# Kernel optimization log

Measured on AMD Instinct MI355X. Metric: run time of the kernel, lower is better.

Reference implementation:

```python
import jax, jax.numpy as jnp
import numpy as np

H = 8  # head_num

def setup_inputs() -> dict:
    key = jax.random.key(0)
    k1, k2, k3, k4, k5 = jax.random.split(key, 5)
    n, e = 4096, 128
    x = jax.random.normal(k1, (n, e), dtype=jnp.float32)
    # torch Linear weights stored here as [in, out]; scale ~ 1/sqrt(fan_in)
    w_qkv = jax.random.normal(k2, (e, e * 3 * H), dtype=jnp.float32) * (1.0 / np.sqrt(e))
    b_qkv = jax.random.normal(k3, (e * 3 * H,), dtype=jnp.float32) * 0.01
    w_proj = jax.random.normal(k4, (e * H, e), dtype=jnp.float32) * (1.0 / np.sqrt(e * H))
    b_proj = jax.random.normal(k5, (e,), dtype=jnp.float32) * 0.01
    return {"x": x, "w_qkv": w_qkv, "b_qkv": b_qkv, "w_proj": w_proj, "b_proj": b_proj}

def reference(x, w_qkv, b_qkv, w_proj, b_proj):
    n, e = x.shape
    # packed layout along output dim is (h, d, qkv) per rearrange 'n (h d qkv) -> qkv h n d'
    qkv = (x @ w_qkv + b_qkv).reshape(n, H, e, 3)          # [n, h, d, 3]
    q = jnp.transpose(qkv[..., 0], (1, 0, 2))              # [h, n, d]
    k = jnp.transpose(qkv[..., 1], (1, 0, 2))
    v = jnp.transpose(qkv[..., 2], (1, 0, 2))
    energy = jnp.einsum('hqd,hkd->hqk', q, k)              # [h, n, n]
    scaling = jnp.asarray(e, x.dtype) ** 0.5
    att = jax.nn.softmax(energy, axis=-1) / scaling        # post-softmax scale (as in source)
    out = jnp.einsum('hqk,hkd->hqd', att, v)               # [h, n, d]
    out = jnp.transpose(out, (1, 0, 2)).reshape(n, H * e)  # [n, h*d]
    return out @ w_proj + b_proj
```

## Files before the change

### kernel.cpp

```cpp
#include <hip/hip_runtime.h>
#include <hip/hip_fp16.h>


#define N_TOK 4096
#define DH 128
#define NH 8

#define EXP2F(x) __builtin_amdgcn_exp2f(x)

typedef _Float16 f16;
typedef __attribute__((ext_vector_type(8))) _Float16 f16x8;
typedef __attribute__((ext_vector_type(2))) __fp16 hf2;
typedef __attribute__((ext_vector_type(4))) float f32x4;

#define GLD16(gsrc, ldst) __builtin_amdgcn_global_load_lds( \
    (const __attribute__((address_space(1))) void*)(gsrc), \
    (__attribute__((address_space(3))) void*)(ldst), 16, 0, 0)

__global__ __launch_bounds__(256) void conv_weights(
    const float* __restrict__ w_proj, const float* __restrict__ w_qkv,
    const float* __restrict__ b_qkv,
    f16* __restrict__ wpT, f16* __restrict__ wqkvT, float* __restrict__ bperm)
{
  int t = blockIdx.x * 256 + threadIdx.x;
  if (t < 131072) {
    int k = t >> 7, col = t & 127;
    wpT[col * 1024 + k] = (f16)w_proj[t];
  } else {
    t -= 131072;
    int k = t / 3072;
    int col = t - k * 3072;
    int hh = col / 384;
    int rem = col - hh * 384;
    int d = rem / 3;
    int s = rem - d * 3;
    int colp = s * 1024 + hh * 128 + d;
    float scale = (s == 0) ? 1.4426950408889634f : 1.0f;
    wqkvT[colp * 128 + k] = (f16)(w_qkv[t] * scale);
    if (k == 0) bperm[colp] = b_qkv[col] * scale;
  }
}

__global__ __launch_bounds__(256) void qkv_gemm2(
    const float* __restrict__ x, const f16* __restrict__ wqkvT,
    const float* __restrict__ bperm,
    f16* __restrict__ Qh, f16* __restrict__ Kh, f16* __restrict__ Vt)
{
  const int cb = blockIdx.x;
  const int rb = blockIdx.y;
  const int tid = threadIdx.x;
  const int w = tid >> 6, lane = tid & 63;
  const int l16 = lane & 15, lhi = lane >> 4;
  const int s = cb >> 3, h = cb & 7;

  f16x8 xf[2][4];
#pragma unroll
  for (int m = 0; m < 2; ++m)
#pragma unroll
    for (int kt = 0; kt < 4; ++kt) {
      const float* xp = x + (size_t)(rb * 128 + w * 32 + m * 16 + l16) * 128 + kt * 32 + lhi * 8;
      f32x4 x0 = *(const f32x4*)xp, x1 = *(const f32x4*)(xp + 4);
      f16x8 v;
#pragma unroll
      for (int j = 0; j < 4; ++j) { v[j] = (f16)x0[j]; v[4 + j] = (f16)x1[j]; }
      xf[m][kt] = v;
    }

  f32x4 acc[8][2];
#pragma unroll
  for (int nt = 0; nt < 8; ++nt)
#pragma unroll
    for (int m = 0; m < 2; ++m) acc[nt][m] = (f32x4){0.f, 0.f, 0.f, 0.f};

#pragma unroll
  for (int nt = 0; nt < 8; ++nt)
#pragma unroll
    for (int kt = 0; kt < 4; ++kt) {
      f16x8 wf = *(const f16x8*)(wqkvT + (size_t)(cb * 128 + nt * 16 + l16) * 128 + kt * 32 + lhi * 8);
      acc[nt][0] = __builtin_amdgcn_mfma_f32_16x16x32_f16(wf, xf[0][kt], acc[nt][0], 0, 0, 0);
      acc[nt][1] = __builtin_amdgcn_mfma_f32_16x16x32_f16(wf, xf[1][kt], acc[nt][1], 0, 0, 0);
    }

#pragma unroll
  for (int nt = 0; nt < 8; ++nt) {
    f32x4 bb = *(const f32x4*)(bperm + cb * 128 + nt * 16 + 4 * lhi);
#pragma unroll
    for (int m = 0; m < 2; ++m) acc[nt][m] += bb;
  }

  if (s == 2) {
#pragma unroll
    for (int nt = 0; nt < 8; ++nt)
#pragma unroll
      for (int m = 0; m < 2; ++m)
#pragma unroll
        for (int r = 0; r < 4; ++r)
          Vt[(size_t)(h * 128 + nt * 16 + 4 * lhi + r) * N_TOK + rb * 128 + w * 32 + m * 16 + l16] =
              (f16)acc[nt][m][r];
  } else {
    __shared__ f16 tr[128][136];
#pragma unroll
    for (int nt = 0; nt < 8; ++nt)
#pragma unroll
      for (int m = 0; m < 2; ++m)
#pragma unroll
        for (int r = 0; r < 4; ++r)
          tr[w * 32 + m * 16 + l16][nt * 16 + 4 * lhi + r] = (f16)acc[nt][m][r];
    __syncthreads();
    f16* dst = (s == 0 ? Qh : Kh) + (size_t)(h * N_TOK + rb * 128) * 128;
    int r = tid >> 1, dh = (tid & 1) * 64;
#pragma unroll
    for (int i = 0; i < 8; ++i)
      *(f16x8*)(dst + r * 128 + dh + i * 8) = *(const f16x8*)(&tr[r][dh + i * 8]);
  }
}

__global__ __launch_bounds__(512, 2) void flash_attn(
    const f16* __restrict__ Qh, const f16* __restrict__ Kh,
    const f16* __restrict__ Vt, f16* __restrict__ opart, float* __restrict__ mlpart)
{
  const int bid = blockIdx.x;
  const int h = bid & 7, sp = (bid >> 3) & 1, qb = bid >> 4;
  const int tid = threadIdx.x;
  const int w = tid >> 6, lane = tid & 63;
  const int l16 = lane & 15, lhi = lane >> 4;

  __shared__ __align__(16) char smem[65536];

  f16x8 qf[2][4];
#pragma unroll
  for (int m = 0; m < 2; ++m)
#pragma unroll
    for (int kt = 0; kt < 4; ++kt)
      qf[m][kt] = *(const f16x8*)(Qh +
          (size_t)(h * N_TOK + qb * 256 + w * 32 + m * 16 + l16) * DH + kt * 32 + lhi * 8);

  int koff[4][4], voff[2][8];
#pragma unroll
  for (int nt = 0; nt < 4; ++nt) {
    int row = 32 * (nt >> 1) + 8 * (l16 >> 2) + 4 * (nt & 1) + (l16 & 3);
    int fk = (row & 3) | ((row & 8) >> 1);
#pragma unroll
    for (int kt = 0; kt < 4; ++kt)
      koff[nt][kt] = row * 256 + ((kt * 4 + lhi) ^ fk) * 16;
  }
#pragma unroll
  for (int ks = 0; ks < 2; ++ks)
#pragma unroll
    for (int dt = 0; dt < 8; ++dt) {
      int rowv = dt * 16 + l16;
      voff[ks][dt] = rowv * 128 + (((ks * 4 + lhi) ^ (rowv & 7))) * 16;
    }

  f32x4 o[2][8];
#pragma unroll
  for (int m = 0; m < 2; ++m)
#pragma unroll
    for (int dt = 0; dt < 8; ++dt) o[m][dt] = (f32x4){0.f, 0.f, 0.f, 0.f};
  float mrun[2] = {-3e38f, -3e38f}, lrun[2] = {0.f, 0.f};

  const f16* Kgh = Kh + (size_t)h * N_TOK * DH;
  const f16* Vgh = Vt + (size_t)h * DH * N_TOK;

  auto stage = [&](int buf, int kb) {
    char* kd = smem + buf * 16384;
    char* vd = smem + 32768 + buf * 16384;
#pragma unroll
    for (int c2 = 0; c2 < 2; ++c2) {
      int c = w * 2 + c2;
      {
        int row = c * 4 + (lane >> 4);
        int fk = (row & 3) | ((row & 8) >> 1);
        const f16* src = Kgh + (size_t)(kb * 64 + row) * DH + ((lane & 15) ^ fk) * 8;
        GLD16(src, kd + c * 1024);
      }
      {
        int row = c * 8 + (lane >> 3);
        const f16* src = Vgh + (size_t)row * N_TOK + kb * 64 + ((lane & 7) ^ (row & 7)) * 8;
        GLD16(src, vd + c * 1024);
      }
    }
  };

  const int kb0 = sp * 32;
  stage(0, kb0);
  asm volatile("s_waitcnt vmcnt(0)" ::: "memory");
  __builtin_amdgcn_sched_barrier(0);
  __builtin_amdgcn_s_barrier();

  int buf = 0;
  for (int kb = kb0; kb < kb0 + 32; ++kb) {
    if (kb < kb0 + 31) {
      stage(buf ^ 1, kb + 1);
      asm volatile("s_waitcnt vmcnt(4)" ::: "memory");
    } else {
      asm volatile("s_waitcnt vmcnt(0)" ::: "memory");
    }
    __builtin_amdgcn_sched_barrier(0);
    __builtin_amdgcn_s_barrier();

    const char* kd = smem + buf * 16384;
    const char* vd = smem + 32768 + buf * 16384;

    f32x4 sv[2][4];
    __builtin_amdgcn_s_setprio(1);
#pragma unroll
    for (int nt = 0; nt < 4; ++nt) {
      f32x4 a0 = {0.f, 0.f, 0.f, 0.f}, a1 = {0.f, 0.f, 0.f, 0.f};
#pragma unroll
      for (int kt = 0; kt < 4; ++kt) {
        f16x8 kf = *(const f16x8*)(kd + koff[nt][kt]);
        a0 = __builtin_amdgcn_mfma_f32_16x16x32_f16(kf, qf[0][kt], a0, 0, 0, 0);
        a1 = __builtin_amdgcn_mfma_f32_16x16x32_f16(kf, qf[1][kt], a1, 0, 0, 0);
      }
      sv[0][nt] = a0; sv[1][nt] = a1;
    }
    __builtin_amdgcn_s_setprio(0);

    f16x8 pf[2][2];
#pragma unroll
    for (int m = 0; m < 2; ++m) {
      f32x4 mv;
#pragma unroll
      for (int r = 0; r < 4; ++r)
        mv[r] = fmaxf(fmaxf(sv[m][0][r], sv[m][1][r]), fmaxf(sv[m][2][r], sv[m][3][r]));
      float pmax = fmaxf(fmaxf(mv[0], mv[1]), fmaxf(mv[2], mv[3]));
      if (!__all(pmax - mrun[m] <= 8.f)) {
        float rm = fmaxf(pmax, __shfl_xor(pmax, 16));
        rm = fmaxf(rm, __shfl_xor(rm, 32));
        float mnew = fmaxf(mrun[m], rm);
        float sc = EXP2F(mrun[m] - mnew);
        lrun[m] *= sc;
#pragma unroll
        for (int dt = 0; dt < 8; ++dt) o[m][dt] *= sc;
        mrun[m] = mnew;
      }
      float mr = mrun[m];
      f32x4 ps = {0.f, 0.f, 0.f, 0.f};
#pragma unroll
      for (int nt = 0; nt < 4; ++nt)
#pragma unroll
        for (int r = 0; r < 4; ++r) {
          float p = EXP2F(sv[m][nt][r] - mr);
          sv[m][nt][r] = p;
          ps[r] += p;
        }
      lrun[m] += (ps[0] + ps[1]) + (ps[2] + ps[3]);
#pragma unroll
      for (int ks = 0; ks < 2; ++ks) {
        union { f16x8 v; hf2 hh[4]; } u;
        u.hh[0] = __builtin_amdgcn_cvt_pkrtz(sv[m][2 * ks][0], sv[m][2 * ks][1]);
        u.hh[1] = __builtin_amdgcn_cvt_pkrtz(sv[m][2 * ks][2], sv[m][2 * ks][3]);
        u.hh[2] = __builtin_amdgcn_cvt_pkrtz(sv[m][2 * ks + 1][0], sv[m][2 * ks + 1][1]);
        u.hh[3] = __builtin_amdgcn_cvt_pkrtz(sv[m][2 * ks + 1][2], sv[m][2 * ks + 1][3]);
        pf[m][ks] = u.v;
      }
    }

    __builtin_amdgcn_s_setprio(1);
#pragma unroll
    for (int ks = 0; ks < 2; ++ks)
#pragma unroll
      for (int dt = 0; dt < 8; ++dt) {
        f16x8 vf = *(const f16x8*)(vd + voff[ks][dt]);
        o[0][dt] = __builtin_amdgcn_mfma_f32_16x16x32_f16(vf, pf[0][ks], o[0][dt], 0, 0, 0);
        o[1][dt] = __builtin_amdgcn_mfma_f32_16x16x32_f16(vf, pf[1][ks], o[1][dt], 0, 0, 0);
      }
    __builtin_amdgcn_s_setprio(0);

    __builtin_amdgcn_s_barrier();
    buf ^= 1;
  }

  f16* ob = opart + ((size_t)((sp * 8 + h) * 16 + qb)) * 32768;
  float* mlb = mlpart + ((size_t)((sp * 8 + h) * 16 + qb)) * 512;
#pragma unroll
  for (int m = 0; m < 2; ++m) {
    float lr = lrun[m];
    lr += __shfl_xor(lr, 16);
    lr += __shfl_xor(lr, 32);
    float rl = 1.0f / lr;
#pragma unroll
    for (int dt = 0; dt < 8; ++dt)
#pragma unroll
      for (int r = 0; r < 4; ++r)
        ob[(dt * 16 + 4 * lhi + r) * 256 + w * 32 + m * 16 + l16] = (f16)(o[m][dt][r] * rl);
    if (lhi == 0) {
      mlb[w * 32 + m * 16 + l16] = mrun[m];
      mlb[256 + w * 32 + m * 16 + l16] = lr;
    }
  }
}

__global__ __launch_bounds__(256) void proj_combine(
    const f16* __restrict__ opart, const float* __restrict__ mlpart,
    const f16* __restrict__ wpT, const float* __restrict__ b_proj,
    float* __restrict__ out)
{
  const int tid = threadIdx.x;
  const int w = tid >> 6;
  const int lane = tid & 63;
  const int l16 = lane & 15, lhi = lane >> 4;
  const int rb = blockIdx.x * 16;
  const int qb = rb >> 8;
  const int nl0 = rb & 255;

  __shared__ f16 A[16][1032];
  __shared__ float wl[8][16][3];
  __shared__ float red[4][16][128];

  const float isc = 0.08838834764831845f;
  if (tid < 128) {
    int hh = tid >> 4, n = tid & 15;
    const float* ml0 = mlpart + ((size_t)((0 + hh) * 16 + qb)) * 512 + nl0 + n;
    const float* ml1 = mlpart + ((size_t)((8 + hh) * 16 + qb)) * 512 + nl0 + n;
    float m0 = ml0[0], l0 = ml0[256], m1 = ml1[0], l1 = ml1[256];
    float mt = fmaxf(m0, m1);
    float n0 = EXP2F(m0 - mt) * l0, n1 = EXP2F(m1 - mt) * l1;
    wl[hh][n][0] = n0; wl[hh][n][1] = n1;
    wl[hh][n][2] = isc / (n0 + n1);
  }
  __syncthreads();

  {
    int d = tid >> 1, nn = (tid & 1) * 8;
#pragma unroll
    for (int hh = 0; hh < 8; ++hh) {
      const f16* O0 = opart + ((size_t)((0 + hh) * 16 + qb)) * 32768 + d * 256 + nl0 + nn;
      const f16* O1 = opart + ((size_t)((8 + hh) * 16 + qb)) * 32768 + d * 256 + nl0 + nn;
      f16x8 a0 = *(const f16x8*)O0, a1 = *(const f16x8*)O1;
#pragma unroll
      for (int j = 0; j < 8; ++j) {
        int n = nn + j;
        float v = ((float)a0[j] * wl[hh][n][0] + (float)a1[j] * wl[hh][n][1]) * wl[hh][n][2];
        A[n][hh * 128 + d] = (f16)v;
      }
    }
  }
  __syncthreads();

  f32x4 o[8];
#pragma unroll
  for (int dt = 0; dt < 8; ++dt) o[dt] = (f32x4){0.f, 0.f, 0.f, 0.f};

#pragma unroll
  for (int kb = 0; kb < 8; ++kb) {
    int k0 = w * 256 + kb * 32 + lhi * 8;
    f16x8 a = *(const f16x8*)(&A[l16][k0]);
#pragma unroll
    for (int dt = 0; dt < 8; ++dt) {
      f16x8 b = *(const f16x8*)(wpT + (size_t)(dt * 16 + l16) * 1024 + k0);
      o[dt] = __builtin_amdgcn_mfma_f32_16x16x32_f16(a, b, o[dt], 0, 0, 0);
    }
  }

#pragma unroll
  for (int dt = 0; dt < 8; ++dt)
#pragma unroll
    for (int r = 0; r < 4; ++r)
      red[w][lhi * 4 + r][dt * 16 + l16] = o[dt][r];
  __syncthreads();
#pragma unroll
  for (int i = 0; i < 8; ++i) {
    int idx = tid + 256 * i;
    int row = idx >> 7, col = idx & 127;
    float v = red[0][row][col] + red[1][row][col] + red[2][row][col]
            + red[3][row][col] + b_proj[col];
    out[(size_t)(rb + row) * 128 + col] = v;
  }
}

extern "C" void kernel_launch(void* const* d_in, const int* in_sizes, int n_in,
                              void* d_out, int out_size, void* d_ws, size_t ws_size,
                              hipStream_t stream) {
  const float* x      = (const float*)d_in[0];
  const float* w_qkv  = (const float*)d_in[1];
  const float* b_qkv  = (const float*)d_in[2];
  const float* w_proj = (const float*)d_in[3];
  const float* b_proj = (const float*)d_in[4];
  float* out = (float*)d_out;

  char* ws = (char*)d_ws;
  const size_t MB = 1024 * 1024;
  f16*   Qh     = (f16*)(ws);
  f16*   Kh     = (f16*)(ws + 8 * MB);
  f16*   Vt     = (f16*)(ws + 16 * MB);
  f16*   opart  = (f16*)(ws + 24 * MB);
  float* mlpart = (float*)(ws + 40 * MB);
  f16*   wpT    = (f16*)(ws + 40 * MB + 512 * 1024);
  f16*   wqkvT  = (f16*)(ws + 40 * MB + 768 * 1024);
  float* bperm  = (float*)(ws + 41 * MB + 512 * 1024);

  hipLaunchKernelGGL(conv_weights, dim3(2048), dim3(256), 0, stream,
                     w_proj, w_qkv, b_qkv, wpT, wqkvT, bperm);
  hipLaunchKernelGGL(qkv_gemm2, dim3(24, 32), dim3(256), 0, stream,
                     x, wqkvT, bperm, Qh, Kh, Vt);
  hipLaunchKernelGGL(flash_attn, dim3(256), dim3(512), 0, stream,
                     Qh, Kh, Vt, opart, mlpart);
  hipLaunchKernelGGL(proj_combine, dim3(256), dim3(256), 0, stream,
                     opart, mlpart, wpT, b_proj, out);
}
```

Baseline: 137.1 us.

## Split attention KV range four ways and trade double buffering for occupancy

The flash attention kernel now splits the key range into four chunks instead of two, doubling the grid to 512 blocks. It drops the double-buffered LDS pipeline for a single 32 KB buffer with plain syncthreads, and raises the launch-bounds occupancy hint from 2 to 4, so more blocks share a CU and hide latency instead of explicit prefetch. The projection/combine kernel merges four partial softmax results instead of two, and the workspace layout grows to hold the larger partial output. The risks are register pressure or spills under the tighter occupancy hint, no load/compute overlap within a block, and extra partial traffic in the combine step.

```diff
diff --git a/kernel.cpp b/kernel.cpp
--- a/kernel.cpp
+++ b/kernel.cpp
@@ -115,17 +115,17 @@
   }
 }
 
-__global__ __launch_bounds__(512, 2) void flash_attn(
+__global__ __launch_bounds__(512, 4) void flash_attn(
     const f16* __restrict__ Qh, const f16* __restrict__ Kh,
     const f16* __restrict__ Vt, f16* __restrict__ opart, float* __restrict__ mlpart)
 {
   const int bid = blockIdx.x;
-  const int h = bid & 7, sp = (bid >> 3) & 1, qb = bid >> 4;
+  const int h = bid & 7, sp = (bid >> 3) & 3, qb = bid >> 5;
   const int tid = threadIdx.x;
   const int w = tid >> 6, lane = tid & 63;
   const int l16 = lane & 15, lhi = lane >> 4;
 
-  __shared__ __align__(16) char smem[65536];
+  __shared__ __align__(16) char smem[32768];
 
   f16x8 qf[2][4];
 #pragma unroll
@@ -162,9 +162,9 @@
   const f16* Kgh = Kh + (size_t)h * N_TOK * DH;
   const f16* Vgh = Vt + (size_t)h * DH * N_TOK;
 
-  auto stage = [&](int buf, int kb) {
-    char* kd = smem + buf * 16384;
-    char* vd = smem + 32768 + buf * 16384;
+  auto stage = [&](int kb) {
+    char* kd = smem;
+    char* vd = smem + 16384;
 #pragma unroll
     for (int c2 = 0; c2 < 2; ++c2) {
       int c = w * 2 + c2;
@@ -182,25 +182,13 @@
     }
   };
 
-  const int kb0 = sp * 32;
-  stage(0, kb0);
-  asm volatile("s_waitcnt vmcnt(0)" ::: "memory");
-  __builtin_amdgcn_sched_barrier(0);
-  __builtin_amdgcn_s_barrier();
-
-  int buf = 0;
-  for (int kb = kb0; kb < kb0 + 32; ++kb) {
-    if (kb < kb0 + 31) {
-      stage(buf ^ 1, kb + 1);
-      asm volatile("s_waitcnt vmcnt(4)" ::: "memory");
-    } else {
-      asm volatile("s_waitcnt vmcnt(0)" ::: "memory");
-    }
-    __builtin_amdgcn_sched_barrier(0);
-    __builtin_amdgcn_s_barrier();
-
-    const char* kd = smem + buf * 16384;
-    const char* vd = smem + 32768 + buf * 16384;
+  const int kb0 = sp * 16;
+  const char* kd = smem;
+  const char* vd = smem + 16384;
+
+  for (int it = 0; it < 16; ++it) {
+    stage(kb0 + it);
+    __syncthreads();
 
     f32x4 sv[2][4];
     __builtin_amdgcn_s_setprio(1);
@@ -268,8 +256,7 @@
       }
     __builtin_amdgcn_s_setprio(0);
 
-    __builtin_amdgcn_s_barrier();
-    buf ^= 1;
+    __syncthreads();
   }
 
   f16* ob = opart + ((size_t)((sp * 8 + h) * 16 + qb)) * 32768;
@@ -306,19 +293,25 @@
   const int nl0 = rb & 255;
 
   __shared__ f16 A[16][1032];
-  __shared__ float wl[8][16][3];
+  __shared__ float wl[8][16][4];
   __shared__ float red[4][16][128];
 
   const float isc = 0.08838834764831845f;
   if (tid < 128) {
     int hh = tid >> 4, n = tid & 15;
-    const float* ml0 = mlpart + ((size_t)((0 + hh) * 16 + qb)) * 512 + nl0 + n;
-    const float* ml1 = mlpart + ((size_t)((8 + hh) * 16 + qb)) * 512 + nl0 + n;
-    float m0 = ml0[0], l0 = ml0[256], m1 = ml1[0], l1 = ml1[256];
-    float mt = fmaxf(m0, m1);
-    float n0 = EXP2F(m0 - mt) * l0, n1 = EXP2F(m1 - mt) * l1;
-    wl[hh][n][0] = n0; wl[hh][n][1] = n1;
-    wl[hh][n][2] = isc / (n0 + n1);
+    float mi[4], li[4];
+#pragma unroll
+    for (int i = 0; i < 4; ++i) {
+      const float* ml = mlpart + ((size_t)((i * 8 + hh) * 16 + qb)) * 512 + nl0 + n;
+      mi[i] = ml[0]; li[i] = ml[256];
+    }
+    float mt = fmaxf(fmaxf(mi[0], mi[1]), fmaxf(mi[2], mi[3]));
+    float ni[4], tot = 0.f;
+#pragma unroll
+    for (int i = 0; i < 4; ++i) { ni[i] = EXP2F(mi[i] - mt) * li[i]; tot += ni[i]; }
+    float rl = isc / tot;
+#pragma unroll
+    for (int i = 0; i < 4; ++i) wl[hh][n][i] = ni[i] * rl;
   }
   __syncthreads();
 
@@ -326,15 +319,16 @@
     int d = tid >> 1, nn = (tid & 1) * 8;
 #pragma unroll
     for (int hh = 0; hh < 8; ++hh) {
-      const f16* O0 = opart + ((size_t)((0 + hh) * 16 + qb)) * 32768 + d * 256 + nl0 + nn;
-      const f16* O1 = opart + ((size_t)((8 + hh) * 16 + qb)) * 32768 + d * 256 + nl0 + nn;
-      f16x8 a0 = *(const f16x8*)O0, a1 = *(const f16x8*)O1;
-#pragma unroll
-      for (int j = 0; j < 8; ++j) {
-        int n = nn + j;
-        float v = ((float)a0[j] * wl[hh][n][0] + (float)a1[j] * wl[hh][n][1]) * wl[hh][n][2];
-        A[n][hh * 128 + d] = (f16)v;
-      }
+      float sum[8] = {};
+#pragma unroll
+      for (int i = 0; i < 4; ++i) {
+        const f16* Oi = opart + ((size_t)((i * 8 + hh) * 16 + qb)) * 32768 + d * 256 + nl0 + nn;
+        f16x8 a = *(const f16x8*)Oi;
+#pragma unroll
+        for (int j = 0; j < 8; ++j) sum[j] += (float)a[j] * wl[hh][nn + j][i];
+      }
+#pragma unroll
+      for (int j = 0; j < 8; ++j) A[nn + j][hh * 128 + d] = (f16)sum[j];
     }
   }
   __syncthreads();
@@ -386,16 +380,16 @@
   f16*   Kh     = (f16*)(ws + 8 * MB);
   f16*   Vt     = (f16*)(ws + 16 * MB);
   f16*   opart  = (f16*)(ws + 24 * MB);
-  float* mlpart = (float*)(ws + 40 * MB);
-  f16*   wpT    = (f16*)(ws + 40 * MB + 512 * 1024);
-  f16*   wqkvT  = (f16*)(ws + 40 * MB + 768 * 1024);
-  float* bperm  = (float*)(ws + 41 * MB + 512 * 1024);
+  float* mlpart = (float*)(ws + 56 * MB);
+  f16*   wpT    = (f16*)(ws + 57 * MB);
+  f16*   wqkvT  = (f16*)(ws + 57 * MB + 256 * 1024);
+  float* bperm  = (float*)(ws + 58 * MB);
 
   hipLaunchKernelGGL(conv_weights, dim3(2048), dim3(256), 0, stream,
                      w_proj, w_qkv, b_qkv, wpT, wqkvT, bperm);
   hipLaunchKernelGGL(qkv_gemm2, dim3(24, 32), dim3(256), 0, stream,
                      x, wqkvT, bperm, Qh, Kh, Vt);
-  hipLaunchKernelGGL(flash_attn, dim3(256), dim3(512), 0, stream,
+  hipLaunchKernelGGL(flash_attn, dim3(512), dim3(512), 0, stream,
                      Qh, Kh, Vt, opart, mlpart);
   hipLaunchKernelGGL(proj_combine, dim3(256), dim3(256), 0, stream,
                      opart, mlpart, wpT, b_proj, out);
```

Result: slower. 313.0 us (+128.3%).

## Halve flash attention query tile and pack LDS offsets into 16-bit pairs

Applied to the files above, without the earlier changes.

The attention kernel now uses 256-thread blocks covering 128 query rows, launched as 512 blocks, and each wave stages twice as many K/V chunks. The K and V LDS offsets are packed two per register to cut VGPR pressure. The hand-placed vmcnt waits and barriers become plain __syncthreads. The combine kernel and the partial-output layout are updated to the new tile size, and the normalization scale is folded into the per-row weights. The aim is more, smaller blocks for scheduling and lower register use, at the cost of reloading K/V once per smaller query tile and extra shift/mask work to unpack offsets.

```diff
diff --git a/kernel.cpp b/kernel.cpp
--- a/kernel.cpp
+++ b/kernel.cpp
@@ -115,7 +115,7 @@
   }
 }
 
-__global__ __launch_bounds__(512, 2) void flash_attn(
+__global__ __launch_bounds__(256, 2) void flash_attn(
     const f16* __restrict__ Qh, const f16* __restrict__ Kh,
     const f16* __restrict__ Vt, f16* __restrict__ opart, float* __restrict__ mlpart)
 {
@@ -133,23 +133,28 @@
 #pragma unroll
     for (int kt = 0; kt < 4; ++kt)
       qf[m][kt] = *(const f16x8*)(Qh +
-          (size_t)(h * N_TOK + qb * 256 + w * 32 + m * 16 + l16) * DH + kt * 32 + lhi * 8);
-
-  int koff[4][4], voff[2][8];
+          (size_t)(h * N_TOK + qb * 128 + w * 32 + m * 16 + l16) * DH + kt * 32 + lhi * 8);
+
+  int koffp[8], voffp[8];
 #pragma unroll
   for (int nt = 0; nt < 4; ++nt) {
     int row = 32 * (nt >> 1) + 8 * (l16 >> 2) + 4 * (nt & 1) + (l16 & 3);
     int fk = (row & 3) | ((row & 8) >> 1);
-#pragma unroll
-    for (int kt = 0; kt < 4; ++kt)
-      koff[nt][kt] = row * 256 + ((kt * 4 + lhi) ^ fk) * 16;
+    int k0 = row * 256 + ((0 + lhi) ^ fk) * 16;
+    int k1 = row * 256 + ((4 + lhi) ^ fk) * 16;
+    int k2 = row * 256 + ((8 + lhi) ^ fk) * 16;
+    int k3 = row * 256 + ((12 + lhi) ^ fk) * 16;
+    koffp[nt * 2 + 0] = k0 | (k1 << 16);
+    koffp[nt * 2 + 1] = k2 | (k3 << 16);
   }
 #pragma unroll
   for (int ks = 0; ks < 2; ++ks)
 #pragma unroll
-    for (int dt = 0; dt < 8; ++dt) {
-      int rowv = dt * 16 + l16;
-      voff[ks][dt] = rowv * 128 + (((ks * 4 + lhi) ^ (rowv & 7))) * 16;
+    for (int d2 = 0; d2 < 4; ++d2) {
+      int r0 = (d2 * 2) * 16 + l16, r1 = (d2 * 2 + 1) * 16 + l16;
+      int v0 = r0 * 128 + (((ks * 4 + lhi) ^ (r0 & 7)) * 16);
+      int v1 = r1 * 128 + (((ks * 4 + lhi) ^ (r1 & 7)) * 16);
+      voffp[ks * 4 + d2] = v0 | (v1 << 16);
     }
 
   f32x4 o[2][8];
@@ -166,8 +171,8 @@
     char* kd = smem + buf * 16384;
     char* vd = smem + 32768 + buf * 16384;
 #pragma unroll
-    for (int c2 = 0; c2 < 2; ++c2) {
-      int c = w * 2 + c2;
+    for (int c4 = 0; c4 < 4; ++c4) {
+      int c = w * 4 + c4;
       {
         int row = c * 4 + (lane >> 4);
         int fk = (row & 3) | ((row & 8) >> 1);
@@ -184,21 +189,10 @@
 
   const int kb0 = sp * 32;
   stage(0, kb0);
-  asm volatile("s_waitcnt vmcnt(0)" ::: "memory");
-  __builtin_amdgcn_sched_barrier(0);
-  __builtin_amdgcn_s_barrier();
-
+  __syncthreads();
   int buf = 0;
   for (int kb = kb0; kb < kb0 + 32; ++kb) {
-    if (kb < kb0 + 31) {
-      stage(buf ^ 1, kb + 1);
-      asm volatile("s_waitcnt vmcnt(4)" ::: "memory");
-    } else {
-      asm volatile("s_waitcnt vmcnt(0)" ::: "memory");
-    }
-    __builtin_amdgcn_sched_barrier(0);
-    __builtin_amdgcn_s_barrier();
-
+    if (kb < kb0 + 31) stage(buf ^ 1, kb + 1);
     const char* kd = smem + buf * 16384;
     const char* vd = smem + 32768 + buf * 16384;
 
@@ -209,7 +203,9 @@
       f32x4 a0 = {0.f, 0.f, 0.f, 0.f}, a1 = {0.f, 0.f, 0.f, 0.f};
 #pragma unroll
       for (int kt = 0; kt < 4; ++kt) {
-        f16x8 kf = *(const f16x8*)(kd + koff[nt][kt]);
+        int ko = (kt & 1) ? (int)((unsigned)koffp[nt * 2 + (kt >> 1)] >> 16)
+                          : (koffp[nt * 2 + (kt >> 1)] & 0xffff);
+        f16x8 kf = *(const f16x8*)(kd + ko);
         a0 = __builtin_amdgcn_mfma_f32_16x16x32_f16(kf, qf[0][kt], a0, 0, 0, 0);
         a1 = __builtin_amdgcn_mfma_f32_16x16x32_f16(kf, qf[1][kt], a1, 0, 0, 0);
       }
@@ -241,9 +237,9 @@
       for (int nt = 0; nt < 4; ++nt)
 #pragma unroll
         for (int r = 0; r < 4; ++r) {
-          float p = EXP2F(sv[m][nt][r] - mr);
-          sv[m][nt][r] = p;
-          ps[r] += p;
+          float pv = EXP2F(sv[m][nt][r] - mr);
+          sv[m][nt][r] = pv;
+          ps[r] += pv;
         }
       lrun[m] += (ps[0] + ps[1]) + (ps[2] + ps[3]);
 #pragma unroll
@@ -262,18 +258,20 @@
     for (int ks = 0; ks < 2; ++ks)
 #pragma unroll
       for (int dt = 0; dt < 8; ++dt) {
-        f16x8 vf = *(const f16x8*)(vd + voff[ks][dt]);
+        int vo = (dt & 1) ? (int)((unsigned)voffp[ks * 4 + (dt >> 1)] >> 16)
+                          : (voffp[ks * 4 + (dt >> 1)] & 0xffff);
+        f16x8 vf = *(const f16x8*)(vd + vo);
         o[0][dt] = __builtin_amdgcn_mfma_f32_16x16x32_f16(vf, pf[0][ks], o[0][dt], 0, 0, 0);
         o[1][dt] = __builtin_amdgcn_mfma_f32_16x16x32_f16(vf, pf[1][ks], o[1][dt], 0, 0, 0);
       }
     __builtin_amdgcn_s_setprio(0);
 
-    __builtin_amdgcn_s_barrier();
+    __syncthreads();
     buf ^= 1;
   }
 
-  f16* ob = opart + ((size_t)((sp * 8 + h) * 16 + qb)) * 32768;
-  float* mlb = mlpart + ((size_t)((sp * 8 + h) * 16 + qb)) * 512;
+  f16* ob = opart + ((size_t)((sp * 8 + h) * 32 + qb)) * 16384;
+  float* mlb = mlpart + ((size_t)((sp * 8 + h) * 32 + qb)) * 256;
 #pragma unroll
   for (int m = 0; m < 2; ++m) {
     float lr = lrun[m];
@@ -284,10 +282,10 @@
     for (int dt = 0; dt < 8; ++dt)
 #pragma unroll
       for (int r = 0; r < 4; ++r)
-        ob[(dt * 16 + 4 * lhi + r) * 256 + w * 32 + m * 16 + l16] = (f16)(o[m][dt][r] * rl);
+        ob[(dt * 16 + 4 * lhi + r) * 128 + w * 32 + m * 16 + l16] = (f16)(o[m][dt][r] * rl);
     if (lhi == 0) {
       mlb[w * 32 + m * 16 + l16] = mrun[m];
-      mlb[256 + w * 32 + m * 16 + l16] = lr;
+      mlb[128 + w * 32 + m * 16 + l16] = lr;
     }
   }
 }
@@ -302,23 +300,24 @@
   const int lane = tid & 63;
   const int l16 = lane & 15, lhi = lane >> 4;
   const int rb = blockIdx.x * 16;
-  const int qb = rb >> 8;
-  const int nl0 = rb & 255;
+  const int qb = rb >> 7;
+  const int nl0 = rb & 127;
 
   __shared__ f16 A[16][1032];
-  __shared__ float wl[8][16][3];
+  __shared__ float wl[8][16][2];
   __shared__ float red[4][16][128];
 
   const float isc = 0.08838834764831845f;
   if (tid < 128) {
     int hh = tid >> 4, n = tid & 15;
-    const float* ml0 = mlpart + ((size_t)((0 + hh) * 16 + qb)) * 512 + nl0 + n;
-    const float* ml1 = mlpart + ((size_t)((8 + hh) * 16 + qb)) * 512 + nl0 + n;
-    float m0 = ml0[0], l0 = ml0[256], m1 = ml1[0], l1 = ml1[256];
+    const float* ml0 = mlpart + ((size_t)((0 + hh) * 32 + qb)) * 256 + nl0 + n;
+    const float* ml1 = mlpart + ((size_t)((8 + hh) * 32 + qb)) * 256 + nl0 + n;
+    float m0 = ml0[0], l0 = ml0[128], m1 = ml1[0], l1 = ml1[128];
     float mt = fmaxf(m0, m1);
     float n0 = EXP2F(m0 - mt) * l0, n1 = EXP2F(m1 - mt) * l1;
-    wl[hh][n][0] = n0; wl[hh][n][1] = n1;
-    wl[hh][n][2] = isc / (n0 + n1);
+    float rl = isc / (n0 + n1);
+    wl[hh][n][0] = n0 * rl;
+    wl[hh][n][1] = n1 * rl;
   }
   __syncthreads();
 
@@ -326,13 +325,13 @@
     int d = tid >> 1, nn = (tid & 1) * 8;
 #pragma unroll
     for (int hh = 0; hh < 8; ++hh) {
-      const f16* O0 = opart + ((size_t)((0 + hh) * 16 + qb)) * 32768 + d * 256 + nl0 + nn;
-      const f16* O1 = opart + ((size_t)((8 + hh) * 16 + qb)) * 32768 + d * 256 + nl0 + nn;
+      const f16* O0 = opart + ((size_t)((0 + hh) * 32 + qb)) * 16384 + d * 128 + nl0 + nn;
+      const f16* O1 = opart + ((size_t)((8 + hh) * 32 + qb)) * 16384 + d * 128 + nl0 + nn;
       f16x8 a0 = *(const f16x8*)O0, a1 = *(const f16x8*)O1;
 #pragma unroll
       for (int j = 0; j < 8; ++j) {
         int n = nn + j;
-        float v = ((float)a0[j] * wl[hh][n][0] + (float)a1[j] * wl[hh][n][1]) * wl[hh][n][2];
+        float v = (float)a0[j] * wl[hh][n][0] + (float)a1[j] * wl[hh][n][1];
         A[n][hh * 128 + d] = (f16)v;
       }
     }
@@ -395,7 +394,7 @@
                      w_proj, w_qkv, b_qkv, wpT, wqkvT, bperm);
   hipLaunchKernelGGL(qkv_gemm2, dim3(24, 32), dim3(256), 0, stream,
                      x, wqkvT, bperm, Qh, Kh, Vt);
-  hipLaunchKernelGGL(flash_attn, dim3(256), dim3(512), 0, stream,
+  hipLaunchKernelGGL(flash_attn, dim3(512), dim3(256), 0, stream,
                      Qh, Kh, Vt, opart, mlpart);
   hipLaunchKernelGGL(proj_combine, dim3(256), dim3(256), 0, stream,
                      opart, mlpart, wpT, b_proj, out);
```

Result: faster. 133.9 us (-2.3%).
